# Kernel tuning notes

Hardware: AMD Instinct MI355X
Metric: run time of the kernel (lower is better)

## Reference

```python
import jax, jax.numpy as jnp
import numpy as np

EPS = 1e-5
TAU = 0.1

def _bn(x, g, b):
    # BatchNorm1d in training mode: batch statistics (biased variance)
    mu = jnp.mean(x, axis=0, keepdims=True)
    var = jnp.var(x, axis=0, keepdims=True)
    return (x - mu) * jax.lax.rsqrt(var + EPS) * g + b

def setup_inputs():
    key = jax.random.key(0)
    ks = jax.random.split(key, 8)
    B, D, H, L, P, C, ND, NP = 32768, 2048, 1024, 384, 192, 10, 2, 2
    s = 0.02
    u = jax.random.uniform(ks[7], (B, NP), minval=1e-6, maxval=1.0 - 1e-6)
    return {
        'x': jax.random.normal(ks[0], (B, D), dtype=jnp.float32),
        'W_pre': jax.random.normal(ks[1], (H, D), dtype=jnp.float32) * s,
        'b_pre': jnp.zeros((H,), jnp.float32),
        'g_pre': jnp.ones((H,), jnp.float32),
        'be_pre': jnp.zeros((H,), jnp.float32),
        'W_disc': jax.random.normal(ks[2], (L, H), dtype=jnp.float32) * s,
        'b_disc': jnp.zeros((L,), jnp.float32),
        'g_disc': jnp.ones((L,), jnp.float32),
        'be_disc': jnp.zeros((L,), jnp.float32),
        'W_dfc': jax.random.normal(ks[3], (ND, L), dtype=jnp.float32) * s,
        'b_dfc': jnp.zeros((ND,), jnp.float32),
        'W_sw': jax.random.normal(ks[4], (NP, L), dtype=jnp.float32) * s,
        'b_sw': jnp.zeros((NP,), jnp.float32),
        'W1': jax.random.normal(ks[5], (NP, P, H), dtype=jnp.float32) * s,
        'b1': jnp.zeros((NP, P), jnp.float32),
        'W2': jax.random.normal(ks[6], (NP, C, P), dtype=jnp.float32) * s,
        'b2': jnp.zeros((NP, C), jnp.float32),
        'gumbel_noise': -jnp.log(-jnp.log(u)),
    }

def reference(x, W_pre, b_pre, g_pre, be_pre, W_disc, b_disc, g_disc, be_disc,
              W_dfc, b_dfc, W_sw, b_sw, W1, b1, W2, b2, gumbel_noise):
    # pre_classifier: Linear + BN + ReLU
    feature = jax.nn.relu(_bn(x @ W_pre.T + b_pre, g_pre, be_pre))
    # GRL is identity in forward
    dp = jax.nn.relu(_bn(feature @ W_disc.T + b_disc, g_disc, be_disc))
    dom = dp @ W_dfc.T + b_dfc                      # [B, num_domains]
    sw = jax.nn.relu(dp @ W_sw.T + b_sw)            # [B, n_partition]
    gum = jax.nn.softmax((sw + gumbel_noise) / TAU, axis=-1)  # soft gumbel-softmax
    idx = jnp.argmax(gum, axis=-1)                  # [B] routing decision
    # compute both (tiny) experts densely, then select per sample (faithful math,
    # avoids per-sample gather of full weight matrices)
    h_all = jax.nn.relu(jnp.einsum('bd,epd->bep', feature, W1) + b1)  # [B,E,P]
    o_all = jnp.einsum('bep,ecp->bec', h_all, W2) + b2                # [B,E,C]
    out = jnp.take_along_axis(o_all, idx[:, None, None], axis=1)[:, 0]  # [B,C]
    # original: sum_p gum[b,p] * stacked (stacked has one entry) == out * sum(gum)
    cop = out * jnp.sum(gum, axis=-1, keepdims=True)
    return cop, dom, idx
```

## Files before the change

kernel.cpp:

```cpp
#include <hip/hip_runtime.h>
#include <math.h>

#define kB 32768
#define kD 2048
#define kH 1024
#define kL 384
#define kP 192
#define kC 10
#define kNP 2
#define kND 2
#define kNCAT 768
#define kTAU 0.1f
#define kEPS 1e-5f
#define NPART 128
#define RPP (kB / NPART)

#define SCALE 64.0f
#define INV_SC2 (1.0f / 4096.0f)

typedef _Float16 f16x8 __attribute__((ext_vector_type(8)));
typedef _Float16 f16x4 __attribute__((ext_vector_type(4)));
typedef float f32x4 __attribute__((ext_vector_type(4)));

__device__ __forceinline__ void gll16(const unsigned short* g, unsigned short* l)
{
    __builtin_amdgcn_global_load_lds(
        (const __attribute__((address_space(1))) unsigned int*)g,
        (__attribute__((address_space(3))) unsigned int*)l, 16, 0, 0);
}

__global__ __launch_bounds__(256)
void split_pack(const float* __restrict__ in, unsigned short* __restrict__ out, int K)
{
    const int row = blockIdx.x;
    const int t = threadIdx.x;
    const int s = row & 7;
    const float* ir = in + (size_t)row * K;
    unsigned short* orow = out + (size_t)row * (K * 2);
    for (int k0 = t * 4; k0 < K; k0 += 1024) {
        const float4 v = *(const float4*)&ir[k0];
        const float a0 = v.x * SCALE, a1 = v.y * SCALE, a2 = v.z * SCALE, a3 = v.w * SCALE;
        const _Float16 h0 = (_Float16)a0, h1 = (_Float16)a1, h2 = (_Float16)a2, h3 = (_Float16)a3;
        const _Float16 l0 = (_Float16)(a0 - (float)h0), l1 = (_Float16)(a1 - (float)h1);
        const _Float16 l2 = (_Float16)(a2 - (float)h2), l3 = (_Float16)(a3 - (float)h3);
        const f16x4 hi = {h0, h1, h2, h3};
        const f16x4 lo = {l0, l1, l2, l3};
        const int kb = k0 >> 5, kk = k0 & 31;
        const int c = kk >> 3, off = kk & 7;
        *(f16x4*)&orow[kb * 64 + ((c ^ s) << 3) + off]       = hi;
        *(f16x4*)&orow[kb * 64 + (((c ^ 4) ^ s) << 3) + off] = lo;
    }
}

__global__ __launch_bounds__(256)
void split_bn(const float* __restrict__ Z, const float* __restrict__ scl,
              const float* __restrict__ shf, unsigned short* __restrict__ out)
{
    const int row = blockIdx.x;
    const int t = threadIdx.x;
    const int s = row & 7;
    const int k0 = t * 4;
    const float4 v = *(const float4*)&Z[(size_t)row * kH + k0];
    const float4 sc = *(const float4*)&scl[k0];
    const float4 sh = *(const float4*)&shf[k0];
    const float a0 = fmaxf(fmaf(v.x, sc.x, sh.x), 0.f);
    const float a1 = fmaxf(fmaf(v.y, sc.y, sh.y), 0.f);
    const float a2 = fmaxf(fmaf(v.z, sc.z, sh.z), 0.f);
    const float a3 = fmaxf(fmaf(v.w, sc.w, sh.w), 0.f);
    const _Float16 h0 = (_Float16)a0, h1 = (_Float16)a1, h2 = (_Float16)a2, h3 = (_Float16)a3;
    const _Float16 l0 = (_Float16)(a0 - (float)h0), l1 = (_Float16)(a1 - (float)h1);
    const _Float16 l2 = (_Float16)(a2 - (float)h2), l3 = (_Float16)(a3 - (float)h3);
    const f16x4 hi = {h0, h1, h2, h3};
    const f16x4 lo = {l0, l1, l2, l3};
    const int kb = k0 >> 5, kk = k0 & 31;
    const int c = kk >> 3, off = kk & 7;
    unsigned short* orow = out + (size_t)row * 2048;
    *(f16x4*)&orow[kb * 64 + ((c ^ s) << 3) + off]       = hi;
    *(f16x4*)&orow[kb * 64 + (((c ^ 4) ^ s) << 3) + off] = lo;
}

__global__ __launch_bounds__(256, 2)
void gemm_sp(const unsigned short* __restrict__ Apk,
             const unsigned short* __restrict__ Bpk,
             float* __restrict__ C, int N, int nkb)
{
    __shared__ unsigned short As[128 * 64];
    __shared__ unsigned short Bs[128 * 64];
    const int t = threadIdx.x;
    const int lane = t & 63;
    const int w = t >> 6;
    const int wr = w >> 1, wc = w & 1;
    const int lg = lane >> 4, lr = lane & 15, ls = lane & 7;
    const int m0 = blockIdx.y * 128, n0 = blockIdx.x * 128;
    const size_t astride = (size_t)nkb * 64;

    const unsigned short* aG[4];
    const unsigned short* bG[4];
    unsigned short* aL[4];
    unsigned short* bL[4];
#pragma unroll
    for (int it = 0; it < 4; ++it) {
        const int Q = (w * 4 + it) * 64 + lane;
        const int row = Q >> 3, c = Q & 7;
        aG[it] = Apk + (size_t)(m0 + row) * astride + c * 8;
        bG[it] = Bpk + (size_t)(n0 + row) * astride + c * 8;
        aL[it] = &As[(w * 4 + it) * 512];
        bL[it] = &Bs[(w * 4 + it) * 512];
    }

    f32x4 acc[4][4];
#pragma unroll
    for (int mi = 0; mi < 4; ++mi)
#pragma unroll
        for (int ni = 0; ni < 4; ++ni) acc[mi][ni] = (f32x4){0.f, 0.f, 0.f, 0.f};

    const int ca = (lg ^ ls) * 8;

    for (int kb = 0; kb < nkb; ++kb) {
        const size_t ko = (size_t)kb * 64;
#pragma unroll
        for (int it = 0; it < 4; ++it) {
            gll16(aG[it] + ko, aL[it]);
            gll16(bG[it] + ko, bL[it]);
        }
        __syncthreads();

        f16x8 ah[4], al[4], bh[4], bl[4];
#pragma unroll
        for (int mi = 0; mi < 4; ++mi) {
            const int ra = (wr * 64 + mi * 16 + lr) * 64;
            ah[mi] = *(const f16x8*)&As[ra + ca];
            al[mi] = *(const f16x8*)&As[ra + (ca ^ 32)];
            const int rb = (wc * 64 + mi * 16 + lr) * 64;
            bh[mi] = *(const f16x8*)&Bs[rb + ca];
            bl[mi] = *(const f16x8*)&Bs[rb + (ca ^ 32)];
        }
#pragma unroll
        for (int mi = 0; mi < 4; ++mi)
#pragma unroll
            for (int ni = 0; ni < 4; ++ni) {
                acc[mi][ni] = __builtin_amdgcn_mfma_f32_16x16x32_f16(ah[mi], bh[ni], acc[mi][ni], 0, 0, 0);
                acc[mi][ni] = __builtin_amdgcn_mfma_f32_16x16x32_f16(ah[mi], bl[ni], acc[mi][ni], 0, 0, 0);
                acc[mi][ni] = __builtin_amdgcn_mfma_f32_16x16x32_f16(al[mi], bh[ni], acc[mi][ni], 0, 0, 0);
            }
        __syncthreads();
    }

#pragma unroll
    for (int mi = 0; mi < 4; ++mi)
#pragma unroll
        for (int j = 0; j < 4; ++j) {
            const int row = m0 + wr * 64 + mi * 16 + lg * 4 + j;
            float* cr = C + (size_t)row * N + n0 + wc * 64 + lr;
#pragma unroll
            for (int ni = 0; ni < 4; ++ni) cr[ni * 16] = acc[mi][ni][j];
        }
}

__global__ __launch_bounds__(256)
void colstat_partial(const float* __restrict__ Z, int ldz, int ncols,
                     float* __restrict__ psum, float* __restrict__ psumsq)
{
    const int c = blockIdx.x * 256 + threadIdx.x;
    if (c >= ncols) return;
    const float* p = Z + (size_t)blockIdx.y * RPP * ldz + c;
    float s = 0.f, sq = 0.f;
    for (int rr = 0; rr < RPP; ++rr) {
        const float v = p[(size_t)rr * ldz];
        s += v;
        sq = fmaf(v, v, sq);
    }
    psum[(size_t)blockIdx.y * ncols + c]   = s;
    psumsq[(size_t)blockIdx.y * ncols + c] = sq;
}

__global__ __launch_bounds__(256)
void colstat_finalize(const float* __restrict__ psum, const float* __restrict__ psumsq,
                      int ncols, const float* __restrict__ g, const float* __restrict__ be,
                      float* __restrict__ scale, float* __restrict__ shift,
                      float inv_sc, float outsc)
{
    const int c = blockIdx.x * 256 + threadIdx.x;
    if (c >= ncols) return;
    float s = 0.f, sq = 0.f;
    for (int i = 0; i < NPART; ++i) {
        s  += psum[(size_t)i * ncols + c];
        sq += psumsq[(size_t)i * ncols + c];
    }
    const float mup = s * (1.f / kB);
    const float var = (sq * (1.f / kB) - mup * mup) * inv_sc * inv_sc;
    const float scl = outsc * g[c] * rsqrtf(var + kEPS) * inv_sc;
    scale[c] = scl;
    shift[c] = fmaf(-mup, scl, outsc * be[c]);
}

__global__ __launch_bounds__(256)
void tail_kernel(const float* __restrict__ Z2,
                 const float* __restrict__ scale2, const float* __restrict__ shift2,
                 const float* __restrict__ W_dfc, const float* __restrict__ b_dfc,
                 const float* __restrict__ W_sw, const float* __restrict__ b_sw,
                 const float* __restrict__ b1, const float* __restrict__ W2,
                 const float* __restrict__ b2, const float* __restrict__ noise,
                 float* __restrict__ out)
{
    __shared__ float sWdfc[kND * kL];
    __shared__ float sWsw[kNP * kL];
    __shared__ float sW2[kNP * kC * kP];
    __shared__ float sb1[kNP * kP];
    __shared__ float sScale[kL];
    __shared__ float sShift[kL];
    const int t = threadIdx.x;
    for (int i = t; i < kND * kL; i += 256) sWdfc[i] = W_dfc[i];
    for (int i = t; i < kNP * kL; i += 256) sWsw[i] = W_sw[i];
    for (int i = t; i < kNP * kC * kP; i += 256) sW2[i] = W2[i];
    for (int i = t; i < kNP * kP; i += 256) sb1[i] = b1[i];
    for (int i = t; i < kL; i += 256) { sScale[i] = scale2[i]; sShift[i] = shift2[i]; }
    __syncthreads();

    const int lane = t & 63;
    const int b = blockIdx.x * 4 + (t >> 6);
    const float* z = Z2 + (size_t)b * kNCAT;

    float d0 = 0.f, d1 = 0.f, s0 = 0.f, s1 = 0.f;
#pragma unroll
    for (int j = 0; j < 6; ++j) {
        const int k = lane + j * 64;
        const float dp = fmaxf(fmaf(z[k], sScale[k], sShift[k]), 0.f);
        d0 = fmaf(dp, sWdfc[k],      d0);
        d1 = fmaf(dp, sWdfc[kL + k], d1);
        s0 = fmaf(dp, sWsw[k],       s0);
        s1 = fmaf(dp, sWsw[kL + k],  s1);
    }
#pragma unroll
    for (int off = 32; off; off >>= 1) {
        d0 += __shfl_xor(d0, off);
        d1 += __shfl_xor(d1, off);
        s0 += __shfl_xor(s0, off);
        s1 += __shfl_xor(s1, off);
    }
    d0 += b_dfc[0];
    d1 += b_dfc[1];

    const float sw0 = fmaxf(s0 + b_sw[0], 0.f);
    const float sw1 = fmaxf(s1 + b_sw[1], 0.f);
    const float l0 = (sw0 + noise[(size_t)b * 2 + 0]) * (1.f / kTAU);
    const float l1 = (sw1 + noise[(size_t)b * 2 + 1]) * (1.f / kTAU);
    const float mx = fmaxf(l0, l1);
    const float e0 = expf(l0 - mx), e1 = expf(l1 - mx);
    const float inv = 1.f / (e0 + e1);
    const float sgum = e0 * inv + e1 * inv;
    const int idx = (l1 > l0) ? 1 : 0;

    const float* zh = z + kL + idx * kP;
    const float h0 = fmaxf(fmaf(zh[lane],       INV_SC2, sb1[idx * kP + lane]),       0.f);
    const float h1 = fmaxf(fmaf(zh[lane + 64],  INV_SC2, sb1[idx * kP + lane + 64]),  0.f);
    const float h2 = fmaxf(fmaf(zh[lane + 128], INV_SC2, sb1[idx * kP + lane + 128]), 0.f);

    float* cop  = out;
    float* dom  = out + (size_t)kB * kC;
    float* idxo = dom + (size_t)kB * kND;

#pragma unroll
    for (int c = 0; c < kC; ++c) {
        const float* wv = &sW2[(idx * kC + c) * kP];
        float oc = h0 * wv[lane] + h1 * wv[lane + 64] + h2 * wv[lane + 128];
#pragma unroll
        for (int off = 32; off; off >>= 1) oc += __shfl_xor(oc, off);
        if (lane == c) cop[(size_t)b * kC + c] = (oc + b2[idx * kC + c]) * sgum;
    }
    if (lane == 0) {
        dom[(size_t)b * 2 + 0] = d0;
        dom[(size_t)b * 2 + 1] = d1;
        idxo[b] = (float)idx;
    }
}

extern "C" void kernel_launch(void* const* d_in, const int* in_sizes, int n_in,
                              void* d_out, int out_size, void* d_ws, size_t ws_size,
                              hipStream_t stream)
{
    const float* x       = (const float*)d_in[0];
    const float* W_pre   = (const float*)d_in[1];
    const float* g_pre   = (const float*)d_in[3];
    const float* be_pre  = (const float*)d_in[4];
    const float* W_disc  = (const float*)d_in[5];
    const float* g_disc  = (const float*)d_in[7];
    const float* be_disc = (const float*)d_in[8];
    const float* W_dfc   = (const float*)d_in[9];
    const float* b_dfc   = (const float*)d_in[10];
    const float* W_sw    = (const float*)d_in[11];
    const float* b_sw    = (const float*)d_in[12];
    const float* W1      = (const float*)d_in[13];
    const float* b1      = (const float*)d_in[14];
    const float* W2      = (const float*)d_in[15];
    const float* b2      = (const float*)d_in[16];
    const float* noise   = (const float*)d_in[17];

    char* wsb = (char*)d_ws;
    const size_t xs_bytes  = (size_t)kB * (2 * kD) * 2;
    const size_t wps_bytes = (size_t)kH * (2 * kD) * 2;
    const size_t z1_bytes  = (size_t)kB * kH * 4;
    unsigned short* xs  = (unsigned short*)wsb;
    unsigned short* Fs  = xs;
    unsigned short* Wps = (unsigned short*)(wsb + xs_bytes);
    unsigned short* Ws2 = Wps;
    float* Z1 = (float*)(wsb + xs_bytes + wps_bytes);
    float* Z2 = Z1;
    float* psum   = (float*)(wsb + xs_bytes + wps_bytes + z1_bytes);
    float* psumsq = psum + (size_t)NPART * kH;
    float* scale1 = psumsq + (size_t)NPART * kH;
    float* shift1 = scale1 + kH;
    float* scale2 = shift1 + kH;
    float* shift2 = scale2 + kL;
    float* out    = (float*)d_out;

    split_pack<<<dim3(kB), 256, 0, stream>>>(x, xs, kD);
    split_pack<<<dim3(kH), 256, 0, stream>>>(W_pre, Wps, kD);
    gemm_sp<<<dim3(kH / 128, kB / 128), 256, 0, stream>>>(xs, Wps, Z1, kH, kD / 32);
    colstat_partial<<<dim3(kH / 256, NPART), 256, 0, stream>>>(Z1, kH, kH, psum, psumsq);
    colstat_finalize<<<dim3(kH / 256), 256, 0, stream>>>(psum, psumsq, kH, g_pre, be_pre,
                                                         scale1, shift1, INV_SC2, SCALE);
    split_bn<<<dim3(kB), 256, 0, stream>>>(Z1, scale1, shift1, Fs);
    split_pack<<<dim3(kL), 256, 0, stream>>>(W_disc, Ws2, kH);
    split_pack<<<dim3(kNP * kP), 256, 0, stream>>>(W1, Ws2 + (size_t)kL * (2 * kH), kH);
    gemm_sp<<<dim3(kNCAT / 128, kB / 128), 256, 0, stream>>>(Fs, Ws2, Z2, kNCAT, kH / 32);
    colstat_partial<<<dim3(2, NPART), 256, 0, stream>>>(Z2, kNCAT, kL, psum, psumsq);
    colstat_finalize<<<dim3(2), 256, 0, stream>>>(psum, psumsq, kL, g_disc, be_disc,
                                                  scale2, shift2, INV_SC2, 1.0f);
    tail_kernel<<<dim3(kB / 4), 256, 0, stream>>>(Z2, scale2, shift2, W_dfc, b_dfc,
                                                  W_sw, b_sw, b1, W2, b2, noise, out);
}
```

Baseline: 756.4 us.

## Fuse activation split, BN-apply and column stats into double-buffered 256x256 GEMM

Replaces the separate split_pack of x, the split_bn pass and the colstat_partial kernels with one templated GEMM. It loads fp32 activations, applies scaling or BN+ReLU, splits them into hi/lo fp16 in registers and writes them to LDS. It also moves to 256x256 tiles with 512 threads, double-buffered LDS, XCD-aware block remapping, and per-tile column sum/sumsq in the epilogue. This removes large intermediate packed-activation buffers and extra passes over Z1/Z2. The cost is heavier register use, one block per CU, and in-loop conversion work.

```diff
diff --git a/kernel.cpp b/kernel.cpp
--- a/kernel.cpp
+++ b/kernel.cpp
@@ -12,9 +12,7 @@
 #define kNCAT 768
 #define kTAU 0.1f
 #define kEPS 1e-5f
-#define NPART 128
-#define RPP (kB / NPART)
-
+#define NPART 256
 #define SCALE 64.0f
 #define INV_SC2 (1.0f / 4096.0f)
 
@@ -52,126 +50,171 @@
     }
 }
 
-__global__ __launch_bounds__(256)
-void split_bn(const float* __restrict__ Z, const float* __restrict__ scl,
-              const float* __restrict__ shf, unsigned short* __restrict__ out)
-{
-    const int row = blockIdx.x;
-    const int t = threadIdx.x;
-    const int s = row & 7;
-    const int k0 = t * 4;
-    const float4 v = *(const float4*)&Z[(size_t)row * kH + k0];
-    const float4 sc = *(const float4*)&scl[k0];
-    const float4 sh = *(const float4*)&shf[k0];
-    const float a0 = fmaxf(fmaf(v.x, sc.x, sh.x), 0.f);
-    const float a1 = fmaxf(fmaf(v.y, sc.y, sh.y), 0.f);
-    const float a2 = fmaxf(fmaf(v.z, sc.z, sh.z), 0.f);
-    const float a3 = fmaxf(fmaf(v.w, sc.w, sh.w), 0.f);
-    const _Float16 h0 = (_Float16)a0, h1 = (_Float16)a1, h2 = (_Float16)a2, h3 = (_Float16)a3;
-    const _Float16 l0 = (_Float16)(a0 - (float)h0), l1 = (_Float16)(a1 - (float)h1);
-    const _Float16 l2 = (_Float16)(a2 - (float)h2), l3 = (_Float16)(a3 - (float)h3);
-    const f16x4 hi = {h0, h1, h2, h3};
-    const f16x4 lo = {l0, l1, l2, l3};
-    const int kb = k0 >> 5, kk = k0 & 31;
-    const int c = kk >> 3, off = kk & 7;
-    unsigned short* orow = out + (size_t)row * 2048;
-    *(f16x4*)&orow[kb * 64 + ((c ^ s) << 3) + off]       = hi;
-    *(f16x4*)&orow[kb * 64 + (((c ^ 4) ^ s) << 3) + off] = lo;
-}
-
-__global__ __launch_bounds__(256, 2)
-void gemm_sp(const unsigned short* __restrict__ Apk,
-             const unsigned short* __restrict__ Bpk,
-             float* __restrict__ C, int N, int nkb)
-{
-    __shared__ unsigned short As[128 * 64];
-    __shared__ unsigned short Bs[128 * 64];
+template<int KDIM, bool BN>
+__global__ __launch_bounds__(512, 1)
+void gemm_fused(const float* __restrict__ Afp,
+                const unsigned short* __restrict__ Bpk,
+                const float* __restrict__ bnsc, const float* __restrict__ bnsh,
+                float* __restrict__ C, const int N, const int gridX,
+                float* __restrict__ psum, float* __restrict__ psumsq, const int statN)
+{
+    constexpr int NKB = KDIM / 32;
+    __shared__ unsigned short lds[4][256 * 64];
+
     const int t = threadIdx.x;
     const int lane = t & 63;
     const int w = t >> 6;
-    const int wr = w >> 1, wc = w & 1;
-    const int lg = lane >> 4, lr = lane & 15, ls = lane & 7;
-    const int m0 = blockIdx.y * 128, n0 = blockIdx.x * 128;
-    const size_t astride = (size_t)nkb * 64;
-
-    const unsigned short* aG[4];
+    const int wr = w >> 2, wc = w & 3;
+    const int lr = lane & 15, lg = lane >> 4;
+    const int ca = (lg ^ (lr & 7)) * 8;
+
+    const int nwg = gridDim.x;
+    const int chunk = nwg >> 3;
+    const int bid = blockIdx.x;
+    const int logical = (bid & 7) * chunk + (bid >> 3);
+    const int bx = logical % gridX, by = logical / gridX;
+    const int m0 = by * 256, n0 = bx * 256;
+
+    const int arow = t >> 1;
+    const int akh = t & 1;
+    const int s7 = arow & 7;
+    const int c0 = akh * 2, c1 = akh * 2 + 1;
+    const float* aSrc = Afp + (size_t)(m0 + arow) * KDIM + akh * 16;
+
+    const size_t bstride = (size_t)NKB * 64;
     const unsigned short* bG[4];
-    unsigned short* aL[4];
-    unsigned short* bL[4];
+    int bLoff[4];
 #pragma unroll
     for (int it = 0; it < 4; ++it) {
         const int Q = (w * 4 + it) * 64 + lane;
-        const int row = Q >> 3, c = Q & 7;
-        aG[it] = Apk + (size_t)(m0 + row) * astride + c * 8;
-        bG[it] = Bpk + (size_t)(n0 + row) * astride + c * 8;
-        aL[it] = &As[(w * 4 + it) * 512];
-        bL[it] = &Bs[(w * 4 + it) * 512];
-    }
-
-    f32x4 acc[4][4];
-#pragma unroll
-    for (int mi = 0; mi < 4; ++mi)
+        bG[it] = Bpk + (size_t)(n0 + (Q >> 3)) * bstride + (Q & 7) * 8;
+        bLoff[it] = (w * 4 + it) * 512;
+    }
+
+    f32x4 acc[8][4];
+#pragma unroll
+    for (int mi = 0; mi < 8; ++mi)
 #pragma unroll
         for (int ni = 0; ni < 4; ++ni) acc[mi][ni] = (f32x4){0.f, 0.f, 0.f, 0.f};
 
-    const int ca = (lg ^ ls) * 8;
-
-    for (int kb = 0; kb < nkb; ++kb) {
-        const size_t ko = (size_t)kb * 64;
-#pragma unroll
-        for (int it = 0; it < 4; ++it) {
-            gll16(aG[it] + ko, aL[it]);
-            gll16(bG[it] + ko, bL[it]);
-        }
-        __syncthreads();
-
-        f16x8 ah[4], al[4], bh[4], bl[4];
-#pragma unroll
-        for (int mi = 0; mi < 4; ++mi) {
-            const int ra = (wr * 64 + mi * 16 + lr) * 64;
-            ah[mi] = *(const f16x8*)&As[ra + ca];
-            al[mi] = *(const f16x8*)&As[ra + (ca ^ 32)];
-            const int rb = (wc * 64 + mi * 16 + lr) * 64;
-            bh[mi] = *(const f16x8*)&Bs[rb + ca];
-            bl[mi] = *(const f16x8*)&Bs[rb + (ca ^ 32)];
-        }
-#pragma unroll
-        for (int mi = 0; mi < 4; ++mi)
-#pragma unroll
-            for (int ni = 0; ni < 4; ++ni) {
-                acc[mi][ni] = __builtin_amdgcn_mfma_f32_16x16x32_f16(ah[mi], bh[ni], acc[mi][ni], 0, 0, 0);
-                acc[mi][ni] = __builtin_amdgcn_mfma_f32_16x16x32_f16(ah[mi], bl[ni], acc[mi][ni], 0, 0, 0);
-                acc[mi][ni] = __builtin_amdgcn_mfma_f32_16x16x32_f16(al[mi], bh[ni], acc[mi][ni], 0, 0, 0);
+    float4 av[4], scv[4], shv[4];
+
+    auto stage_issue = [&](int kb, int buf) {
+        const int kt = kb * 32;
+#pragma unroll
+        for (int it = 0; it < 4; ++it)
+            gll16(bG[it] + (size_t)kb * 64, &lds[2 + buf][bLoff[it]]);
+#pragma unroll
+        for (int j = 0; j < 4; ++j)
+            av[j] = *(const float4*)&aSrc[kt + j * 4];
+        if constexpr (BN) {
+#pragma unroll
+            for (int j = 0; j < 4; ++j) {
+                scv[j] = *(const float4*)&bnsc[kt + akh * 16 + j * 4];
+                shv[j] = *(const float4*)&bnsh[kt + akh * 16 + j * 4];
             }
-        __syncthreads();
-    }
-
-#pragma unroll
-    for (int mi = 0; mi < 4; ++mi)
+        }
+    };
+
+    auto stage_write = [&](int buf) {
+        float v[16];
 #pragma unroll
         for (int j = 0; j < 4; ++j) {
-            const int row = m0 + wr * 64 + mi * 16 + lg * 4 + j;
+            float4 a = av[j];
+            if constexpr (BN) {
+                a.x = fmaxf(fmaf(a.x, scv[j].x, shv[j].x), 0.f);
+                a.y = fmaxf(fmaf(a.y, scv[j].y, shv[j].y), 0.f);
+                a.z = fmaxf(fmaf(a.z, scv[j].z, shv[j].z), 0.f);
+                a.w = fmaxf(fmaf(a.w, scv[j].w, shv[j].w), 0.f);
+            } else {
+                a.x *= SCALE; a.y *= SCALE; a.z *= SCALE; a.w *= SCALE;
+            }
+            v[j * 4 + 0] = a.x; v[j * 4 + 1] = a.y;
+            v[j * 4 + 2] = a.z; v[j * 4 + 3] = a.w;
+        }
+        f16x8 hi[2], lo[2];
+#pragma unroll
+        for (int h = 0; h < 2; ++h)
+#pragma unroll
+            for (int i = 0; i < 8; ++i) {
+                const float x = v[h * 8 + i];
+                const _Float16 hh = (_Float16)x;
+                hi[h][i] = hh;
+                lo[h][i] = (_Float16)(x - (float)hh);
+            }
+        unsigned short* dst = &lds[buf][arow * 64];
+        *(f16x8*)&dst[(c0 ^ s7) * 8]       = hi[0];
+        *(f16x8*)&dst[(c1 ^ s7) * 8]       = hi[1];
+        *(f16x8*)&dst[((c0 ^ 4) ^ s7) * 8] = lo[0];
+        *(f16x8*)&dst[((c1 ^ 4) ^ s7) * 8] = lo[1];
+    };
+
+    stage_issue(0, 0);
+    stage_write(0);
+    asm volatile("s_waitcnt vmcnt(0) lgkmcnt(0)" ::: "memory");
+    __builtin_amdgcn_s_barrier();
+
+    for (int kb = 0; kb < NKB; ++kb) {
+        const int cur = kb & 1, nxt = cur ^ 1;
+        const bool pf = (kb + 1 < NKB);
+        if (pf) stage_issue(kb + 1, nxt);
+
+        f16x8 bh[4], bl[4];
+#pragma unroll
+        for (int ni = 0; ni < 4; ++ni) {
+            const unsigned short* bb = &lds[2 + cur][(wc * 64 + ni * 16 + lr) * 64];
+            bh[ni] = *(const f16x8*)&bb[ca];
+            bl[ni] = *(const f16x8*)&bb[ca ^ 32];
+        }
+#pragma unroll
+        for (int mi = 0; mi < 8; ++mi) {
+            const unsigned short* ab = &lds[cur][(wr * 128 + mi * 16 + lr) * 64];
+            const f16x8 ah = *(const f16x8*)&ab[ca];
+            const f16x8 al = *(const f16x8*)&ab[ca ^ 32];
+#pragma unroll
+            for (int ni = 0; ni < 4; ++ni)
+                acc[mi][ni] = __builtin_amdgcn_mfma_f32_16x16x32_f16(ah, bh[ni], acc[mi][ni], 0, 0, 0);
+#pragma unroll
+            for (int ni = 0; ni < 4; ++ni)
+                acc[mi][ni] = __builtin_amdgcn_mfma_f32_16x16x32_f16(ah, bl[ni], acc[mi][ni], 0, 0, 0);
+#pragma unroll
+            for (int ni = 0; ni < 4; ++ni)
+                acc[mi][ni] = __builtin_amdgcn_mfma_f32_16x16x32_f16(al, bh[ni], acc[mi][ni], 0, 0, 0);
+        }
+        if (pf) stage_write(nxt);
+        asm volatile("s_waitcnt vmcnt(0) lgkmcnt(0)" ::: "memory");
+        __builtin_amdgcn_s_barrier();
+    }
+
+#pragma unroll
+    for (int mi = 0; mi < 8; ++mi)
+#pragma unroll
+        for (int j = 0; j < 4; ++j) {
+            const int row = m0 + wr * 128 + mi * 16 + lg * 4 + j;
             float* cr = C + (size_t)row * N + n0 + wc * 64 + lr;
 #pragma unroll
             for (int ni = 0; ni < 4; ++ni) cr[ni * 16] = acc[mi][ni][j];
         }
-}
-
-__global__ __launch_bounds__(256)
-void colstat_partial(const float* __restrict__ Z, int ldz, int ncols,
-                     float* __restrict__ psum, float* __restrict__ psumsq)
-{
-    const int c = blockIdx.x * 256 + threadIdx.x;
-    if (c >= ncols) return;
-    const float* p = Z + (size_t)blockIdx.y * RPP * ldz + c;
-    float s = 0.f, sq = 0.f;
-    for (int rr = 0; rr < RPP; ++rr) {
-        const float v = p[(size_t)rr * ldz];
-        s += v;
-        sq = fmaf(v, v, sq);
-    }
-    psum[(size_t)blockIdx.y * ncols + c]   = s;
-    psumsq[(size_t)blockIdx.y * ncols + c] = sq;
+
+#pragma unroll
+    for (int ni = 0; ni < 4; ++ni) {
+        float s = 0.f, sq = 0.f;
+#pragma unroll
+        for (int mi = 0; mi < 8; ++mi)
+#pragma unroll
+            for (int j = 0; j < 4; ++j) {
+                const float v = acc[mi][ni][j];
+                s += v;
+                sq = fmaf(v, v, sq);
+            }
+        s  += __shfl_xor(s, 16);  s  += __shfl_xor(s, 32);
+        sq += __shfl_xor(sq, 16); sq += __shfl_xor(sq, 32);
+        const int col = n0 + wc * 64 + ni * 16 + lr;
+        if (lane < 16 && col < statN) {
+            psum[(size_t)(by * 2 + wr) * statN + col]   = s;
+            psumsq[(size_t)(by * 2 + wr) * statN + col] = sq;
+        }
+    }
 }
 
 __global__ __launch_bounds__(256)
@@ -297,36 +340,31 @@
     const float* noise   = (const float*)d_in[17];
 
     char* wsb = (char*)d_ws;
-    const size_t xs_bytes  = (size_t)kB * (2 * kD) * 2;
-    const size_t wps_bytes = (size_t)kH * (2 * kD) * 2;
-    const size_t z1_bytes  = (size_t)kB * kH * 4;
-    unsigned short* xs  = (unsigned short*)wsb;
-    unsigned short* Fs  = xs;
-    unsigned short* Wps = (unsigned short*)(wsb + xs_bytes);
-    unsigned short* Ws2 = Wps;
-    float* Z1 = (float*)(wsb + xs_bytes + wps_bytes);
-    float* Z2 = Z1;
-    float* psum   = (float*)(wsb + xs_bytes + wps_bytes + z1_bytes);
-    float* psumsq = psum + (size_t)NPART * kH;
-    float* scale1 = psumsq + (size_t)NPART * kH;
+    unsigned short* Wps = (unsigned short*)wsb;
+    unsigned short* Ws2 = (unsigned short*)(wsb + (size_t)1024 * 4096 * 2);
+    float* Z1 = (float*)(wsb + (size_t)1024 * 4096 * 2 + (size_t)768 * 2048 * 2);
+    float* Z2 = Z1 + (size_t)kB * kH;
+    float* psum1  = Z2 + (size_t)kB * kNCAT;
+    float* psq1   = psum1 + (size_t)NPART * kH;
+    float* psum2  = psq1 + (size_t)NPART * kH;
+    float* psq2   = psum2 + (size_t)NPART * kL;
+    float* scale1 = psq2 + (size_t)NPART * kL;
     float* shift1 = scale1 + kH;
     float* scale2 = shift1 + kH;
     float* shift2 = scale2 + kL;
     float* out    = (float*)d_out;
 
-    split_pack<<<dim3(kB), 256, 0, stream>>>(x, xs, kD);
     split_pack<<<dim3(kH), 256, 0, stream>>>(W_pre, Wps, kD);
-    gemm_sp<<<dim3(kH / 128, kB / 128), 256, 0, stream>>>(xs, Wps, Z1, kH, kD / 32);
-    colstat_partial<<<dim3(kH / 256, NPART), 256, 0, stream>>>(Z1, kH, kH, psum, psumsq);
-    colstat_finalize<<<dim3(kH / 256), 256, 0, stream>>>(psum, psumsq, kH, g_pre, be_pre,
-                                                         scale1, shift1, INV_SC2, SCALE);
-    split_bn<<<dim3(kB), 256, 0, stream>>>(Z1, scale1, shift1, Fs);
     split_pack<<<dim3(kL), 256, 0, stream>>>(W_disc, Ws2, kH);
     split_pack<<<dim3(kNP * kP), 256, 0, stream>>>(W1, Ws2 + (size_t)kL * (2 * kH), kH);
-    gemm_sp<<<dim3(kNCAT / 128, kB / 128), 256, 0, stream>>>(Fs, Ws2, Z2, kNCAT, kH / 32);
-    colstat_partial<<<dim3(2, NPART), 256, 0, stream>>>(Z2, kNCAT, kL, psum, psumsq);
-    colstat_finalize<<<dim3(2), 256, 0, stream>>>(psum, psumsq, kL, g_disc, be_disc,
-                                                  scale2, shift2, INV_SC2, 1.0f);
+    gemm_fused<kD, false><<<dim3(4 * 128), 512, 0, stream>>>(
+        x, Wps, nullptr, nullptr, Z1, kH, 4, psum1, psq1, kH);
+    colstat_finalize<<<dim3(kH / 256), 256, 0, stream>>>(psum1, psq1, kH, g_pre, be_pre,
+                                                         scale1, shift1, INV_SC2, SCALE);
+    gemm_fused<kH, true><<<dim3(3 * 128), 512, 0, stream>>>(
+        Z1, Ws2, scale1, shift1, Z2, kNCAT, 3, psum2, psq2, kL);
+    colstat_finalize<<<dim3((kL + 255) / 256), 256, 0, stream>>>(psum2, psq2, kL, g_disc, be_disc,
+                                                                 scale2, shift2, INV_SC2, 1.0f);
     tail_kernel<<<dim3(kB / 4), 256, 0, stream>>>(Z2, scale2, shift2, W_dfc, b_dfc,
                                                   W_sw, b_sw, b1, W2, b2, noise, out);
 }
```

Measured after the change: 650.5 us. 1.16x faster.
